# Kernel tuning notes

Measured on AMD Instinct MI355X. Metric: run time of the kernel, lower is better.

Reference implementation:

```python
import jax, jax.numpy as jnp
import numpy as np

B, C, H, W = 4, 256, 64, 64
CK = C // 8  # query/key channels per OUT_RATIO=8


def setup_inputs() -> dict:
    key = jax.random.key(0)
    ks = jax.random.split(key, 8)
    s_in = 1.0 / np.sqrt(C)
    return {
        "x": jax.random.normal(ks[0], (B, C, H, W), dtype=jnp.float32),
        "Wq": jax.random.uniform(ks[1], (CK, C), jnp.float32, -s_in, s_in),
        "bq": jax.random.uniform(ks[2], (CK,), jnp.float32, -s_in, s_in),
        "Wk": jax.random.uniform(ks[3], (CK, C), jnp.float32, -s_in, s_in),
        "bk": jax.random.uniform(ks[4], (CK,), jnp.float32, -s_in, s_in),
        "Wv": jax.random.uniform(ks[5], (C, C), jnp.float32, -s_in, s_in),
        "bv": jax.random.uniform(ks[6], (C,), jnp.float32, -s_in, s_in),
        "gamma": jnp.zeros((1,), dtype=jnp.float32),
    }


def reference(x, Wq, bq, Wk, bk, Wv, bv, gamma):
    b, c, h, w = x.shape
    n = h * w
    xf = x.reshape(b, c, n)  # [B, C, N]
    # 1x1 convs are channel matmuls
    q = jnp.einsum('oc,bcn->bno', Wq, xf) + bq  # [B, N, CK]
    k = jnp.einsum('oc,bcn->bon', Wk, xf) + bk[None, :, None]  # [B, CK, N]
    v = jnp.einsum('oc,bcn->bon', Wv, xf) + bv[None, :, None]  # [B, C, N]
    energy = jnp.einsum('bno,bom->bnm', q, k)  # [B, N, N], unscaled
    attn = jax.nn.softmax(energy, axis=-1)
    out = jnp.einsum('bcm,bnm->bcn', v, attn)  # [B, C, N]
    out = out.reshape(b, c, h, w)
    return gamma[0] * out + x
```

## Files before the change

kernel.cpp:

```cpp
#include <hip/hip_runtime.h>
#include <math.h>


#define BB 4
#define CC 256
#define NN 4096
#define CKK 32
#define LOG2E 1.44269504f

typedef __attribute__((ext_vector_type(4))) float f32x4;
typedef __attribute__((ext_vector_type(16))) float f32x16;
typedef __attribute__((ext_vector_type(8))) short short8;
typedef __attribute__((ext_vector_type(4))) short short4v;

static __device__ __forceinline__ ushort f2bf(float f) {
    union { float f; unsigned u; } v; v.f = f;
    unsigned r = v.u + 0x7FFFu + ((v.u >> 16) & 1u);
    return (ushort)(r >> 16);
}
static __device__ __forceinline__ float bf2f(ushort h) {
    union { unsigned u; float f; } v; v.u = ((unsigned)h) << 16;
    return v.f;
}
static __device__ __forceinline__ unsigned pack2(float lo, float hi) {
    unsigned r;
    asm("v_cvt_pk_bf16_f32 %0, %1, %2" : "=v"(r) : "v"(lo), "v"(hi));
    return r;
}
static __device__ __forceinline__ float exp2fast(float x) {
    return __builtin_amdgcn_exp2f(x);
}
static __device__ __forceinline__ float maxcross(float x) {
    float a = x, b = x;
    asm("v_permlane32_swap_b32 %0, %1" : "+v"(a), "+v"(b));
    return fmaxf(a, b);
}
static __device__ __forceinline__ float addcross(float x) {
    float a = x, b = x;
    asm("v_permlane32_swap_b32 %0, %1" : "+v"(a), "+v"(b));
    return a + b;
}
static __device__ __forceinline__ void gload_lds16(const void* g, void* l) {
    __builtin_amdgcn_global_load_lds(
        (const __attribute__((address_space(1))) void*)g,
        (__attribute__((address_space(3))) void*)l, 16, 0, 0);
}

union PU { unsigned u[8]; short8 v[2]; };

static __device__ __forceinline__ void softmax_step(
    const f32x16 s, float& m_i, float& l_p, PU& P, float& al, bool& resc)
{
    float t0 = fmaxf(fmaxf(s[0],  s[1]),  s[2]);
    float t1 = fmaxf(fmaxf(s[3],  s[4]),  s[5]);
    float t2 = fmaxf(fmaxf(s[6],  s[7]),  s[8]);
    float t3 = fmaxf(fmaxf(s[9],  s[10]), s[11]);
    float t4 = fmaxf(fmaxf(s[12], s[13]), s[14]);
    float mx = fmaxf(fmaxf(fmaxf(t0, t1), t2), fmaxf(fmaxf(t3, t4), s[15]));
    mx = maxcross(mx);
    resc = mx > m_i + 8.f;
    const float mn = resc ? mx : m_i;
    al = resc ? exp2fast(m_i - mx) : 1.f;
    float sum0 = 0.f, sum1 = 0.f;
    #pragma unroll
    for (int g2 = 0; g2 < 8; ++g2) {
        const float plo = exp2fast(s[2 * g2]     - mn);
        const float phi = exp2fast(s[2 * g2 + 1] - mn);
        if (g2 & 1) sum1 += plo + phi; else sum0 += plo + phi;
        P.u[g2] = pack2(plo, phi);
    }
    l_p = l_p * al + (sum0 + sum1);
    m_i = mn;
}

static __device__ __forceinline__ void pv_step(
    const ushort* vsub, const PU& P, f32x16 (&acc)[8], int h2, int l31)
{
    #pragma unroll
    for (int cb = 0; cb < 8; ++cb) {
        const short8 A0 = *(const short8*)&vsub[(size_t)h2 * 2048       + (cb * 32 + l31) * 8];
        const short8 A1 = *(const short8*)&vsub[(size_t)(2 + h2) * 2048 + (cb * 32 + l31) * 8];
        acc[cb] = __builtin_amdgcn_mfma_f32_32x32x16_bf16(A0, P.v[0], acc[cb], 0, 0, 0);
        acc[cb] = __builtin_amdgcn_mfma_f32_32x32x16_bf16(A1, P.v[1], acc[cb], 0, 0, 0);
    }
}

__global__ __launch_bounds__(256) void pack_w_kernel(
    const float* __restrict__ Wq, const float* __restrict__ bq,
    const float* __restrict__ Wk, const float* __restrict__ bk,
    const float* __restrict__ Wv, const float* __restrict__ bv,
    ushort* __restrict__ Wb, float* __restrict__ bias)
{
    const int o = blockIdx.x;
    const int c = threadIdx.x;
    const float* src; float bsc;
    if (o < 32)      { src = Wq + o * CC;        bsc = bq[o]; }
    else if (o < 64) { src = Wk + (o - 32) * CC; bsc = bk[o - 32]; }
    else             { src = Wv + (o - 64) * CC; bsc = bv[o - 64]; }
    Wb[o * CC + c] = f2bf(src[c]);
    if (c == 0) bias[o] = bsc;
}

__global__ __launch_bounds__(256) void qkv_mfma_kernel(
    const ushort* __restrict__ Wb, const float* __restrict__ bias,
    const float* __restrict__ x,
    ushort* __restrict__ Q, ushort* __restrict__ Kt, ushort* __restrict__ Vg)
{
    const int b = blockIdx.y, n0 = blockIdx.x * 64;
    const int tid = threadIdx.x;
    const int w = tid >> 6, lane = tid & 63, l15 = lane & 15, q = lane >> 4;

    f32x4 acc[5][4];
    #pragma unroll
    for (int c5 = 0; c5 < 5; ++c5)
        #pragma unroll
        for (int nc = 0; nc < 4; ++nc) acc[c5][nc] = (f32x4)0.f;

    const float* xb = x + (size_t)b * CC * NN + n0;

    #pragma unroll
    for (int ks = 0; ks < 8; ++ks) {
        short8 af[5];
        #pragma unroll
        for (int c5 = 0; c5 < 5; ++c5)
            af[c5] = *(const short8*)&Wb[(w * 80 + c5 * 16 + l15) * CC + ks * 32 + q * 8];
        union { unsigned u[4]; short8 v; } bfu[4];
        #pragma unroll
        for (int nc = 0; nc < 4; ++nc) {
            const float* xp = xb + (size_t)(ks * 32 + q * 8) * NN + nc * 16 + l15;
            bfu[nc].u[0] = pack2(xp[0],              xp[(size_t)NN]);
            bfu[nc].u[1] = pack2(xp[2 * (size_t)NN], xp[3 * (size_t)NN]);
            bfu[nc].u[2] = pack2(xp[4 * (size_t)NN], xp[5 * (size_t)NN]);
            bfu[nc].u[3] = pack2(xp[6 * (size_t)NN], xp[7 * (size_t)NN]);
        }
        #pragma unroll
        for (int c5 = 0; c5 < 5; ++c5)
            #pragma unroll
            for (int nc = 0; nc < 4; ++nc)
                acc[c5][nc] = __builtin_amdgcn_mfma_f32_16x16x32_bf16(af[c5], bfu[nc].v, acc[c5][nc], 0, 0, 0);
    }

    const int kh2b = (l15 >> 2) & 1;
    const int jj   = (l15 & 3) + ((l15 >> 3) << 2);

    #pragma unroll
    for (int c5 = 0; c5 < 5; ++c5) {
        const int o0 = w * 80 + c5 * 16;
        float bia[4];
        #pragma unroll
        for (int r = 0; r < 4; ++r) bia[r] = bias[o0 + q * 4 + r];
        if (o0 >= 64) {
            #pragma unroll
            for (int nc = 0; nc < 4; ++nc) {
                const size_t tbase =
                    ((size_t)b * (NN / 32) + (n0 >> 5) + (nc >> 1)) * 8192
                    + (size_t)(((nc & 1) << 1) + kh2b) * 2048 + jj;
                #pragma unroll
                for (int r = 0; r < 4; ++r) {
                    const int c = o0 - 64 + q * 4 + r;
                    Vg[tbase + c * 8] = f2bf(acc[c5][nc][r] + bia[r]);
                }
            }
        } else {
            ushort* dst = (o0 < 32) ? Q : Kt;
            const float sc = (o0 < 32) ? LOG2E : 1.0f;
            const int oo = (o0 & 31) + q * 4;
            #pragma unroll
            for (int nc = 0; nc < 4; ++nc) {
                short4v h;
                #pragma unroll
                for (int r = 0; r < 4; ++r) h[r] = (short)f2bf((acc[c5][nc][r] + bia[r]) * sc);
                *(short4v*)&dst[((size_t)b * NN + n0 + nc * 16 + l15) * CKK + oo] = h;
            }
        }
    }
}

__global__ __launch_bounds__(256, 2) void attn_mfma_kernel(
    const ushort* __restrict__ Q, const ushort* __restrict__ K,
    const ushort* __restrict__ Vg,
    ushort* __restrict__ Op, float* __restrict__ Mp, float* __restrict__ Lp,
    int G, int NSEG)
{
    __shared__ __align__(16) ushort vs[2][16384];

    const int id = blockIdx.x;
    const int xcd = id & 7, ix = id >> 3;
    const int b = xcd >> 1;
    int g, row;
    if (G == 4) { g = ((xcd & 1) << 1) | (ix & 1); row = ix >> 1; }
    else        { g = xcd & 1;                     row = ix; }
    const int n0 = row * 128;

    const int tid = threadIdx.x;
    const int w = tid >> 6, lane = tid & 63;
    const int l31 = lane & 31, h2 = lane >> 5;
    const int n0w = n0 + w * 32;

    const size_t qrow = ((size_t)b * NN + n0w + l31) * CKK;
    const short8 qB0 = *(const short8*)&Q[qrow + h2 * 8];
    const short8 qB1 = *(const short8*)&Q[qrow + 16 + h2 * 8];

    f32x16 acc[8];
    #pragma unroll
    for (int cb = 0; cb < 8; ++cb) acc[cb] = (f32x16)0.f;
    float m_i = -3.0e38f, l_p = 0.f;

    const int m_start = g * NSEG;
    const int NT = NSEG / 64;
    const ushort* Kb = K + (size_t)b * NN * CKK;
    const char* Vseg = (const char*)Vg
        + ((size_t)b * (NN / 32) + (size_t)(m_start >> 5)) * 16384;

    const int goff = (w << 10) + (lane << 4);
    const int loff = (w << 10);

    PU Pp, Pc; float alp, alc; bool rp, rc;

    #pragma unroll
    for (int i = 0; i < 8; ++i)
        gload_lds16(Vseg + (i << 12) + goff, (char*)&vs[0][0] + (i << 12) + loff);

    short8 kA0 = *(const short8*)&Kb[(size_t)(m_start + l31) * CKK + h2 * 8];
    short8 kA1 = *(const short8*)&Kb[(size_t)(m_start + l31) * CKK + 16 + h2 * 8];
    {
        f32x16 s = __builtin_amdgcn_mfma_f32_32x32x16_bf16(kA0, qB0, (f32x16)0.f, 0, 0, 0);
        s = __builtin_amdgcn_mfma_f32_32x32x16_bf16(kA1, qB1, s, 0, 0, 0);
        const size_t kr = (size_t)(m_start + 32 + l31) * CKK;
        kA0 = *(const short8*)&Kb[kr + h2 * 8];
        kA1 = *(const short8*)&Kb[kr + 16 + h2 * 8];
        softmax_step(s, m_i, l_p, Pp, alp, rp);
    }

    for (int t = 0; t < NT - 1; ++t) {
        __syncthreads();
        const char* Vtn = Vseg + (size_t)(t + 1) * 32768;
        #pragma unroll
        for (int i = 0; i < 8; ++i)
            gload_lds16(Vtn + (i << 12) + goff,
                        (char*)&vs[(t + 1) & 1][0] + (i << 12) + loff);
        const ushort* vb = &vs[t & 1][0];

        {
            f32x16 sn = __builtin_amdgcn_mfma_f32_32x32x16_bf16(kA0, qB0, (f32x16)0.f, 0, 0, 0);
            sn = __builtin_amdgcn_mfma_f32_32x32x16_bf16(kA1, qB1, sn, 0, 0, 0);
            const size_t kr = (size_t)(m_start + (2 * t + 2) * 32 + l31) * CKK;
            kA0 = *(const short8*)&Kb[kr + h2 * 8];
            kA1 = *(const short8*)&Kb[kr + 16 + h2 * 8];
            softmax_step(sn, m_i, l_p, Pc, alc, rc);
            pv_step(vb, Pp, acc, h2, l31);
            if (__any(rc)) {
                #pragma unroll
                for (int cb = 0; cb < 8; ++cb) acc[cb] *= alc;
            }
        }
        {
            f32x16 sn = __builtin_amdgcn_mfma_f32_32x32x16_bf16(kA0, qB0, (f32x16)0.f, 0, 0, 0);
            sn = __builtin_amdgcn_mfma_f32_32x32x16_bf16(kA1, qB1, sn, 0, 0, 0);
            const size_t kr = (size_t)(m_start + (2 * t + 3) * 32 + l31) * CKK;
            kA0 = *(const short8*)&Kb[kr + h2 * 8];
            kA1 = *(const short8*)&Kb[kr + 16 + h2 * 8];
            softmax_step(sn, m_i, l_p, Pp, alp, rp);
            pv_step(vb + 8192, Pc, acc, h2, l31);
            if (__any(rp)) {
                #pragma unroll
                for (int cb = 0; cb < 8; ++cb) acc[cb] *= alp;
            }
        }
    }

    __syncthreads();
    {
        const ushort* vb = &vs[(NT - 1) & 1][0];
        f32x16 sn = __builtin_amdgcn_mfma_f32_32x32x16_bf16(kA0, qB0, (f32x16)0.f, 0, 0, 0);
        sn = __builtin_amdgcn_mfma_f32_32x32x16_bf16(kA1, qB1, sn, 0, 0, 0);
        softmax_step(sn, m_i, l_p, Pc, alc, rc);
        pv_step(vb, Pp, acc, h2, l31);
        if (__any(rc)) {
            #pragma unroll
            for (int cb = 0; cb < 8; ++cb) acc[cb] *= alc;
        }
        pv_step(vb + 8192, Pc, acc, h2, l31);
    }

    const float l = addcross(l_p);
    const float linv = 1.f / l;
    if (h2 == 0) {
        const size_t idx = (size_t)(g * BB + b) * NN + n0w + l31;
        Mp[idx] = m_i;
        Lp[idx] = l;
    }
    ushort* ob = Op + (size_t)(g * BB + b) * CC * NN;
    #pragma unroll
    for (int cb = 0; cb < 8; ++cb)
        #pragma unroll
        for (int r = 0; r < 16; ++r) {
            const int c = cb * 32 + (r & 3) + 8 * (r >> 2) + 4 * h2;
            ob[(size_t)c * NN + n0w + l31] = f2bf(acc[cb][r] * linv);
        }
}

template<int G>
__global__ __launch_bounds__(256) void combine_kernel(
    const ushort* __restrict__ Op, const float* __restrict__ Mp,
    const float* __restrict__ Lp, const float* __restrict__ x,
    const float* __restrict__ gamma, float* __restrict__ out)
{
    const int gid = blockIdx.x * 256 + threadIdx.x;
    const int grp   = gid & (NN / 8 - 1);
    const int rowid = gid >> 9;
    const int b = rowid >> 8;
    const int c = rowid & (CC - 1);
    const int n0 = grp * 8;

    f32x4 mp[G][2], lp[G][2];
    #pragma unroll
    for (int g = 0; g < G; ++g) {
        const size_t base = (size_t)(g * BB + b) * NN + n0;
        mp[g][0] = *(const f32x4*)&Mp[base];
        mp[g][1] = *(const f32x4*)&Mp[base + 4];
        lp[g][0] = *(const f32x4*)&Lp[base];
        lp[g][1] = *(const f32x4*)&Lp[base + 4];
    }
    float wgt[G][8];
    #pragma unroll
    for (int h = 0; h < 2; ++h) {
        #pragma unroll
        for (int j = 0; j < 4; ++j) {
            float M = -3.0e38f;
            #pragma unroll
            for (int g = 0; g < G; ++g) M = fmaxf(M, mp[g][h][j]);
            float ws = 0.f;
            #pragma unroll
            for (int g = 0; g < G; ++g) {
                const float wv = lp[g][h][j] * exp2fast(mp[g][h][j] - M);
                wgt[g][h * 4 + j] = wv;
                ws += wv;
            }
            const float inv = 1.f / ws;
            #pragma unroll
            for (int g = 0; g < G; ++g) wgt[g][h * 4 + j] *= inv;
        }
    }

    short8 opv[G];
    #pragma unroll
    for (int g = 0; g < G; ++g)
        opv[g] = *(const short8*)&Op[((size_t)(g * BB + b) * CC + c) * NN + n0];

    const size_t xbase = ((size_t)b * CC + c) * NN + n0;
    const f32x4 x0 = *(const f32x4*)&x[xbase];
    const f32x4 x1 = *(const f32x4*)&x[xbase + 4];
    const float gm = gamma[0];

    f32x4 o0, o1;
    #pragma unroll
    for (int j = 0; j < 4; ++j) {
        float a = 0.f, bsum = 0.f;
        #pragma unroll
        for (int g = 0; g < G; ++g) {
            a    += wgt[g][j]     * bf2f((ushort)opv[g][j]);
            bsum += wgt[g][4 + j] * bf2f((ushort)opv[g][4 + j]);
        }
        o0[j] = gm * a + x0[j];
        o1[j] = gm * bsum + x1[j];
    }
    *(f32x4*)&out[xbase]     = o0;
    *(f32x4*)&out[xbase + 4] = o1;
}

extern "C" void kernel_launch(void* const* d_in, const int* in_sizes, int n_in,
                              void* d_out, int out_size, void* d_ws, size_t ws_size,
                              hipStream_t stream) {
    const float* x     = (const float*)d_in[0];
    const float* Wq    = (const float*)d_in[1];
    const float* bq    = (const float*)d_in[2];
    const float* Wk    = (const float*)d_in[3];
    const float* bk    = (const float*)d_in[4];
    const float* Wv    = (const float*)d_in[5];
    const float* bv    = (const float*)d_in[6];
    const float* gamma = (const float*)d_in[7];
    float* out = (float*)d_out;

    char* p = (char*)d_ws;
    ushort* Wb   = (ushort*)(p);
    float*  bias = (float*) (p + 163840);
    ushort* Qb   = (ushort*)(p + 165120);
    ushort* Kb   = (ushort*)(p + 1213696);
    ushort* Vc   = (ushort*)(p + 2262272);
    float*  Mpb  = (float*) (p + 10650880);
    float*  Lpb  = (float*) (p + 10913024);
    ushort* Opb  = (ushort*)(p + 11175168);
    const int G = (ws_size >= (size_t)44729600) ? 4 : 2;

    pack_w_kernel<<<dim3(320), 256, 0, stream>>>(Wq, bq, Wk, bk, Wv, bv, Wb, bias);
    qkv_mfma_kernel<<<dim3(NN / 64, BB), 256, 0, stream>>>(Wb, bias, x, Qb, Kb, Vc);
    attn_mfma_kernel<<<dim3(128 * G), 256, 0, stream>>>(Qb, Kb, Vc, Opb, Mpb, Lpb, G, NN / G);
    const int cblocks = BB * CC * (NN / 8) / 256;
    if (G == 4)
        combine_kernel<4><<<dim3(cblocks), 256, 0, stream>>>(Opb, Mpb, Lpb, x, gamma, out);
    else
        combine_kernel<2><<<dim3(cblocks), 256, 0, stream>>>(Opb, Mpb, Lpb, x, gamma, out);
}
```

Before: 85.36 us.

## Split attention work across waves by channel half, halve tiles, raise occupancy

Each attention block now covers 64 query rows instead of 128. Pairs of waves share a 32-row query group, and each wave of the pair accumulates half of the 256 output channels. The V tile staged in LDS per step shrinks to one 32-key chunk, with an extra barrier per step. The occupancy target rises to 4 blocks per CU and the grid doubles. The QKV projection kernel also moves to 32-column tiles with twice as many blocks. The intent is more parallelism and lower register and LDS pressure, at the cost of QK and softmax being computed twice per query group and more synchronisation.

```diff
diff --git a/kernel.cpp b/kernel.cpp
--- a/kernel.cpp
+++ b/kernel.cpp
@@ -73,13 +73,14 @@
     m_i = mn;
 }
 
-static __device__ __forceinline__ void pv_step(
-    const ushort* vsub, const PU& P, f32x16 (&acc)[8], int h2, int l31)
-{
-    #pragma unroll
-    for (int cb = 0; cb < 8; ++cb) {
-        const short8 A0 = *(const short8*)&vsub[(size_t)h2 * 2048       + (cb * 32 + l31) * 8];
-        const short8 A1 = *(const short8*)&vsub[(size_t)(2 + h2) * 2048 + (cb * 32 + l31) * 8];
+static __device__ __forceinline__ void pv4(
+    const ushort* vsub, const PU& P, f32x16 (&acc)[4], int h2, int l31, int cb0)
+{
+    #pragma unroll
+    for (int cb = 0; cb < 4; ++cb) {
+        const int c = (cb0 + cb) * 32 + l31;
+        const short8 A0 = *(const short8*)&vsub[(size_t)h2 * 2048       + c * 8];
+        const short8 A1 = *(const short8*)&vsub[(size_t)(2 + h2) * 2048 + c * 8];
         acc[cb] = __builtin_amdgcn_mfma_f32_32x32x16_bf16(A0, P.v[0], acc[cb], 0, 0, 0);
         acc[cb] = __builtin_amdgcn_mfma_f32_32x32x16_bf16(A1, P.v[1], acc[cb], 0, 0, 0);
     }
@@ -106,15 +107,15 @@
     const float* __restrict__ x,
     ushort* __restrict__ Q, ushort* __restrict__ Kt, ushort* __restrict__ Vg)
 {
-    const int b = blockIdx.y, n0 = blockIdx.x * 64;
+    const int b = blockIdx.y, n0 = blockIdx.x * 32;
     const int tid = threadIdx.x;
     const int w = tid >> 6, lane = tid & 63, l15 = lane & 15, q = lane >> 4;
 
-    f32x4 acc[5][4];
+    f32x4 acc[5][2];
     #pragma unroll
     for (int c5 = 0; c5 < 5; ++c5)
         #pragma unroll
-        for (int nc = 0; nc < 4; ++nc) acc[c5][nc] = (f32x4)0.f;
+        for (int nc = 0; nc < 2; ++nc) acc[c5][nc] = (f32x4)0.f;
 
     const float* xb = x + (size_t)b * CC * NN + n0;
 
@@ -124,9 +125,9 @@
         #pragma unroll
         for (int c5 = 0; c5 < 5; ++c5)
             af[c5] = *(const short8*)&Wb[(w * 80 + c5 * 16 + l15) * CC + ks * 32 + q * 8];
-        union { unsigned u[4]; short8 v; } bfu[4];
-        #pragma unroll
-        for (int nc = 0; nc < 4; ++nc) {
+        union { unsigned u[4]; short8 v; } bfu[2];
+        #pragma unroll
+        for (int nc = 0; nc < 2; ++nc) {
             const float* xp = xb + (size_t)(ks * 32 + q * 8) * NN + nc * 16 + l15;
             bfu[nc].u[0] = pack2(xp[0],              xp[(size_t)NN]);
             bfu[nc].u[1] = pack2(xp[2 * (size_t)NN], xp[3 * (size_t)NN]);
@@ -136,7 +137,7 @@
         #pragma unroll
         for (int c5 = 0; c5 < 5; ++c5)
             #pragma unroll
-            for (int nc = 0; nc < 4; ++nc)
+            for (int nc = 0; nc < 2; ++nc)
                 acc[c5][nc] = __builtin_amdgcn_mfma_f32_16x16x32_bf16(af[c5], bfu[nc].v, acc[c5][nc], 0, 0, 0);
     }
 
@@ -151,10 +152,10 @@
         for (int r = 0; r < 4; ++r) bia[r] = bias[o0 + q * 4 + r];
         if (o0 >= 64) {
             #pragma unroll
-            for (int nc = 0; nc < 4; ++nc) {
+            for (int nc = 0; nc < 2; ++nc) {
                 const size_t tbase =
-                    ((size_t)b * (NN / 32) + (n0 >> 5) + (nc >> 1)) * 8192
-                    + (size_t)(((nc & 1) << 1) + kh2b) * 2048 + jj;
+                    ((size_t)b * (NN / 32) + (n0 >> 5)) * 8192
+                    + (size_t)((nc << 1) + kh2b) * 2048 + jj;
                 #pragma unroll
                 for (int r = 0; r < 4; ++r) {
                     const int c = o0 - 64 + q * 4 + r;
@@ -166,7 +167,7 @@
             const float sc = (o0 < 32) ? LOG2E : 1.0f;
             const int oo = (o0 & 31) + q * 4;
             #pragma unroll
-            for (int nc = 0; nc < 4; ++nc) {
+            for (int nc = 0; nc < 2; ++nc) {
                 short4v h;
                 #pragma unroll
                 for (int r = 0; r < 4; ++r) h[r] = (short)f2bf((acc[c5][nc][r] + bia[r]) * sc);
@@ -176,13 +177,13 @@
     }
 }
 
-__global__ __launch_bounds__(256, 2) void attn_mfma_kernel(
+__global__ __launch_bounds__(256, 4) void attn_mfma_kernel(
     const ushort* __restrict__ Q, const ushort* __restrict__ K,
     const ushort* __restrict__ Vg,
     ushort* __restrict__ Op, float* __restrict__ Mp, float* __restrict__ Lp,
     int G, int NSEG)
 {
-    __shared__ __align__(16) ushort vs[2][16384];
+    __shared__ __align__(16) ushort vs[2][8192];
 
     const int id = blockIdx.x;
     const int xcd = id & 7, ix = id >> 3;
@@ -190,24 +191,26 @@
     int g, row;
     if (G == 4) { g = ((xcd & 1) << 1) | (ix & 1); row = ix >> 1; }
     else        { g = xcd & 1;                     row = ix; }
-    const int n0 = row * 128;
+    const int n0 = row * 64;
 
     const int tid = threadIdx.x;
     const int w = tid >> 6, lane = tid & 63;
     const int l31 = lane & 31, h2 = lane >> 5;
-    const int n0w = n0 + w * 32;
+    const int ng = w >> 1, ch = w & 1;
+    const int cb0 = ch * 4;
+    const int n0w = n0 + ng * 32;
 
     const size_t qrow = ((size_t)b * NN + n0w + l31) * CKK;
     const short8 qB0 = *(const short8*)&Q[qrow + h2 * 8];
     const short8 qB1 = *(const short8*)&Q[qrow + 16 + h2 * 8];
 
-    f32x16 acc[8];
-    #pragma unroll
-    for (int cb = 0; cb < 8; ++cb) acc[cb] = (f32x16)0.f;
+    f32x16 acc[4];
+    #pragma unroll
+    for (int cb = 0; cb < 4; ++cb) acc[cb] = (f32x16)0.f;
     float m_i = -3.0e38f, l_p = 0.f;
 
     const int m_start = g * NSEG;
-    const int NT = NSEG / 64;
+    const int NT = NSEG / 32;
     const ushort* Kb = K + (size_t)b * NN * CKK;
     const char* Vseg = (const char*)Vg
         + ((size_t)b * (NN / 32) + (size_t)(m_start >> 5)) * 16384;
@@ -218,7 +221,7 @@
     PU Pp, Pc; float alp, alc; bool rp, rc;
 
     #pragma unroll
-    for (int i = 0; i < 8; ++i)
+    for (int i = 0; i < 4; ++i)
         gload_lds16(Vseg + (i << 12) + goff, (char*)&vs[0][0] + (i << 12) + loff);
 
     short8 kA0 = *(const short8*)&Kb[(size_t)(m_start + l31) * CKK + h2 * 8];
@@ -232,70 +235,76 @@
         softmax_step(s, m_i, l_p, Pp, alp, rp);
     }
 
-    for (int t = 0; t < NT - 1; ++t) {
+    for (int t = 0; t < NT - 2; t += 2) {
         __syncthreads();
-        const char* Vtn = Vseg + (size_t)(t + 1) * 32768;
-        #pragma unroll
-        for (int i = 0; i < 8; ++i)
-            gload_lds16(Vtn + (i << 12) + goff,
-                        (char*)&vs[(t + 1) & 1][0] + (i << 12) + loff);
-        const ushort* vb = &vs[t & 1][0];
-
         {
+            const char* Vn = Vseg + (size_t)(t + 1) * 16384;
+            #pragma unroll
+            for (int i = 0; i < 4; ++i)
+                gload_lds16(Vn + (i << 12) + goff, (char*)&vs[1][0] + (i << 12) + loff);
             f32x16 sn = __builtin_amdgcn_mfma_f32_32x32x16_bf16(kA0, qB0, (f32x16)0.f, 0, 0, 0);
             sn = __builtin_amdgcn_mfma_f32_32x32x16_bf16(kA1, qB1, sn, 0, 0, 0);
-            const size_t kr = (size_t)(m_start + (2 * t + 2) * 32 + l31) * CKK;
+            const size_t kr = (size_t)(m_start + (t + 2) * 32 + l31) * CKK;
             kA0 = *(const short8*)&Kb[kr + h2 * 8];
             kA1 = *(const short8*)&Kb[kr + 16 + h2 * 8];
             softmax_step(sn, m_i, l_p, Pc, alc, rc);
-            pv_step(vb, Pp, acc, h2, l31);
+            pv4(&vs[0][0], Pp, acc, h2, l31, cb0);
             if (__any(rc)) {
                 #pragma unroll
-                for (int cb = 0; cb < 8; ++cb) acc[cb] *= alc;
+                for (int cb = 0; cb < 4; ++cb) acc[cb] *= alc;
             }
         }
+        __syncthreads();
         {
+            const char* Vn = Vseg + (size_t)(t + 2) * 16384;
+            #pragma unroll
+            for (int i = 0; i < 4; ++i)
+                gload_lds16(Vn + (i << 12) + goff, (char*)&vs[0][0] + (i << 12) + loff);
             f32x16 sn = __builtin_amdgcn_mfma_f32_32x32x16_bf16(kA0, qB0, (f32x16)0.f, 0, 0, 0);
             sn = __builtin_amdgcn_mfma_f32_32x32x16_bf16(kA1, qB1, sn, 0, 0, 0);
-            const size_t kr = (size_t)(m_start + (2 * t + 3) * 32 + l31) * CKK;
+            const size_t kr = (size_t)(m_start + (t + 3) * 32 + l31) * CKK;
             kA0 = *(const short8*)&Kb[kr + h2 * 8];
             kA1 = *(const short8*)&Kb[kr + 16 + h2 * 8];
             softmax_step(sn, m_i, l_p, Pp, alp, rp);
-            pv_step(vb + 8192, Pc, acc, h2, l31);
+            pv4(&vs[1][0], Pc, acc, h2, l31, cb0);
             if (__any(rp)) {
                 #pragma unroll
-                for (int cb = 0; cb < 8; ++cb) acc[cb] *= alp;
+                for (int cb = 0; cb < 4; ++cb) acc[cb] *= alp;
             }
         }
     }
 
     __syncthreads();
     {
-        const ushort* vb = &vs[(NT - 1) & 1][0];
+        const char* Vn = Vseg + (size_t)(NT - 1) * 16384;
+        #pragma unroll
+        for (int i = 0; i < 4; ++i)
+            gload_lds16(Vn + (i << 12) + goff, (char*)&vs[1][0] + (i << 12) + loff);
         f32x16 sn = __builtin_amdgcn_mfma_f32_32x32x16_bf16(kA0, qB0, (f32x16)0.f, 0, 0, 0);
         sn = __builtin_amdgcn_mfma_f32_32x32x16_bf16(kA1, qB1, sn, 0, 0, 0);
         softmax_step(sn, m_i, l_p, Pc, alc, rc);
-        pv_step(vb, Pp, acc, h2, l31);
+        pv4(&vs[0][0], Pp, acc, h2, l31, cb0);
         if (__any(rc)) {
             #pragma unroll
-            for (int cb = 0; cb < 8; ++cb) acc[cb] *= alc;
-        }
-        pv_step(vb + 8192, Pc, acc, h2, l31);
-    }
+            for (int cb = 0; cb < 4; ++cb) acc[cb] *= alc;
+        }
+    }
+    __syncthreads();
+    pv4(&vs[1][0], Pc, acc, h2, l31, cb0);
 
     const float l = addcross(l_p);
     const float linv = 1.f / l;
-    if (h2 == 0) {
+    if (ch == 0 && h2 == 0) {
         const size_t idx = (size_t)(g * BB + b) * NN + n0w + l31;
         Mp[idx] = m_i;
         Lp[idx] = l;
     }
     ushort* ob = Op + (size_t)(g * BB + b) * CC * NN;
     #pragma unroll
-    for (int cb = 0; cb < 8; ++cb)
+    for (int cb = 0; cb < 4; ++cb)
         #pragma unroll
         for (int r = 0; r < 16; ++r) {
-            const int c = cb * 32 + (r & 3) + 8 * (r >> 2) + 4 * h2;
+            const int c = (cb0 + cb) * 32 + (r & 3) + 8 * (r >> 2) + 4 * h2;
             ob[(size_t)c * NN + n0w + l31] = f2bf(acc[cb][r] * linv);
         }
 }
@@ -394,8 +403,8 @@
     const int G = (ws_size >= (size_t)44729600) ? 4 : 2;
 
     pack_w_kernel<<<dim3(320), 256, 0, stream>>>(Wq, bq, Wk, bk, Wv, bv, Wb, bias);
-    qkv_mfma_kernel<<<dim3(NN / 64, BB), 256, 0, stream>>>(Wb, bias, x, Qb, Kb, Vc);
-    attn_mfma_kernel<<<dim3(128 * G), 256, 0, stream>>>(Qb, Kb, Vc, Opb, Mpb, Lpb, G, NN / G);
+    qkv_mfma_kernel<<<dim3(NN / 32, BB), 256, 0, stream>>>(Wb, bias, x, Qb, Kb, Vc);
+    attn_mfma_kernel<<<dim3(64 * BB * G), 256, 0, stream>>>(Qb, Kb, Vc, Opb, Mpb, Lpb, G, NN / G);
     const int cblocks = BB * CC * (NN / 8) / 256;
     if (G == 4)
         combine_kernel<4><<<dim3(cblocks), 256, 0, stream>>>(Opb, Mpb, Lpb, x, gamma, out);
```

New measurement: 129.2 us. +51.3%, slower.
